# Kernel optimization log

Hardware: AMD Instinct MI355X
Metric: run time of the kernel (lower is better)

Reference implementation:

```python
import jax, jax.numpy as jnp
import numpy as np

S, H, NUM_TAG, D_LEN, MAX_LEN = 256, 1024, 20, 10, 1000


def setup_inputs() -> dict:
    key = jax.random.key(0)
    ks = jax.random.split(key, 6)
    sc = lambda d: 1.0 / np.sqrt(d)
    return {
        "hidden": jax.random.normal(ks[0], (S, H), jnp.float32),
        "target": jax.random.randint(ks[1], (S,), 0, NUM_TAG),
        "attn_w1": jax.random.normal(ks[2], (H, H), jnp.float32) * sc(H),
        "attn_b1": jnp.zeros((H,), jnp.float32),
        "attn_w2": jax.random.normal(ks[3], (H, 1), jnp.float32) * sc(H),
        "attn_b2": jnp.zeros((1,), jnp.float32),
        "len_emb": jax.random.normal(ks[4], (MAX_LEN, D_LEN), jnp.float32),
        "fc_w": jax.random.normal(ks[5], (3 * H + D_LEN, NUM_TAG), jnp.float32) * sc(3 * H + D_LEN),
        "fc_b": jnp.zeros((NUM_TAG,), jnp.float32),
    }


def reference(hidden, target, attn_w1, attn_b1, attn_w2, attn_b2, len_emb, fc_w, fc_b):
    S_, H_ = hidden.shape
    # attention scores [S]
    a = (jnp.tanh(hidden @ attn_w1 + attn_b1) @ attn_w2 + attn_b2)[:, 0]
    # prefix sums for contiguous-window softmax pooling
    e = jnp.exp(a - jnp.max(a))                                   # [S]
    Zc = jnp.concatenate([jnp.zeros((1,), e.dtype), jnp.cumsum(e)])                      # [S+1]
    Pc = jnp.concatenate([jnp.zeros((1, H_), e.dtype), jnp.cumsum(e[:, None] * hidden, axis=0)])  # [S+1,H]
    ii, jj = jnp.triu_indices(S_, k=1)                            # all spans i<j, loop order
    span = (Pc[jj + 1] - Pc[ii]) / (Zc[jj + 1] - Zc[ii])[:, None]  # softmax-weighted pooling
    lemb = len_emb[jj - ii + 1]                                   # segment length embedding (no grad in torch)
    feats = jnp.concatenate([span, hidden[ii], hidden[jj], lemb], axis=-1)  # [P, 3H+10]
    logits = feats @ fc_w + fc_b                                  # [P, num_tag]
    # is_span labels via run ids
    change = jnp.concatenate([jnp.array([True]), target[1:] != target[:-1]])
    run_id = jnp.cumsum(change.astype(jnp.int32))
    start = change
    end = jnp.concatenate([target[:-1] != target[1:], jnp.array([True])])
    labels = jnp.where((run_id[ii] == run_id[jj]) & start[ii] & end[jj], target[jj], 0)
    logp = jax.nn.log_softmax(logits, axis=-1)
    loss = -jnp.mean(jnp.take_along_axis(logp, labels[:, None].astype(jnp.int32), axis=1))
    return logits, loss.reshape(1)
```

## Files before the change

### kernel.cpp

```cpp
#include <hip/hip_runtime.h>
#include <math.h>

#define S 256
#define H 1024
#define NTAG 20
#define NPAIR 32640

#define WS_T     0
#define WS_A     2097152
#define WS_E     2097408
#define WS_ZC    2097664
#define WS_HW0   2097924
#define WS_HW1   2103044
#define WS_HW2   2108164
#define WS_PW    2113284
#define WS_LW    2118424
#define WS_LOSSP 2123564
#define WS_RUN   2123820
#define WS_START 2124076
#define WS_END   2124332

__global__ __launch_bounds__(256) void kA1(const float* __restrict__ hidden,
                                           const float* __restrict__ w1,
                                           float* __restrict__ ws) {
    const int tid = threadIdx.x;
    const int cg = blockIdx.x;
    const int rg = blockIdx.y;
    const int kc = blockIdx.z;

    __shared__ __align__(16) float shH[128][16];

    const int kk = tid & 127;
    const int r0 = (tid >> 7) * 8;
    #pragma unroll
    for (int e = 0; e < 8; e++)
        shH[kk][r0 + e] = hidden[(rg * 16 + r0 + e) * H + kc * 128 + kk];
    __syncthreads();

    float acc[16];
    #pragma unroll
    for (int r = 0; r < 16; r++) acc[r] = 0.f;

    const float* wp = w1 + (size_t)(kc * 128) * H + cg * 256 + tid;
    #pragma unroll 4
    for (int k = 0; k < 128; k++) {
        const float wv = wp[k * H];
        const float4 h0 = *(const float4*)&shH[k][0];
        const float4 h1 = *(const float4*)&shH[k][4];
        const float4 h2 = *(const float4*)&shH[k][8];
        const float4 h3 = *(const float4*)&shH[k][12];
        acc[0]  = fmaf(h0.x, wv, acc[0]);  acc[1]  = fmaf(h0.y, wv, acc[1]);
        acc[2]  = fmaf(h0.z, wv, acc[2]);  acc[3]  = fmaf(h0.w, wv, acc[3]);
        acc[4]  = fmaf(h1.x, wv, acc[4]);  acc[5]  = fmaf(h1.y, wv, acc[5]);
        acc[6]  = fmaf(h1.z, wv, acc[6]);  acc[7]  = fmaf(h1.w, wv, acc[7]);
        acc[8]  = fmaf(h2.x, wv, acc[8]);  acc[9]  = fmaf(h2.y, wv, acc[9]);
        acc[10] = fmaf(h2.z, wv, acc[10]); acc[11] = fmaf(h2.w, wv, acc[11]);
        acc[12] = fmaf(h3.x, wv, acc[12]); acc[13] = fmaf(h3.y, wv, acc[13]);
        acc[14] = fmaf(h3.z, wv, acc[14]); acc[15] = fmaf(h3.w, wv, acc[15]);
    }

    float* op = ws + WS_T + kc * (S * H) + (rg * 16) * H + cg * 256 + tid;
    #pragma unroll
    for (int r = 0; r < 16; r++) op[r * H] = acc[r];
}

__global__ __launch_bounds__(256) void kA2C(const float* __restrict__ hidden,
                                            const float* __restrict__ b1,
                                            const float* __restrict__ w2,
                                            const float* __restrict__ fcw,
                                            const float* __restrict__ lenemb,
                                            float* __restrict__ ws) {
    const int b = blockIdx.x;
    const int tid = threadIdx.x;
    if (b < 256) {
        __shared__ float hrow[1024];
        __shared__ float part[12][20];
        __shared__ float sred[256];

        #pragma unroll
        for (int e = 0; e < 4; e++)
            hrow[tid + e * 256] = hidden[b * H + tid + e * 256];

        float lacc = 0.f;
        #pragma unroll
        for (int q = 0; q < 4; q++) {
            const int c = q * 256 + tid;
            float sum = 0.f;
            #pragma unroll
            for (int kcz = 0; kcz < 8; kcz++)
                sum += ws[WS_T + kcz * (S * H) + b * H + c];
            lacc += tanhf(sum + b1[c]) * w2[c];
        }
        sred[tid] = lacc;
        __syncthreads();
        for (int off = 128; off > 0; off >>= 1) {
            if (tid < off) sred[tid] += sred[tid + off];
            __syncthreads();
        }
        if (tid == 0) ws[WS_A + b] = sred[0];

        if (tid < 240) {
            const int t = tid % 20, g = tid / 20;
            const int p = g >> 2, kc = g & 3;
            const float* fw = fcw + ((p << 10) + (kc << 8)) * 20 + t;
            const float* hr = hrow + (kc << 8);
            float sacc = 0.f;
            #pragma unroll 8
            for (int k = 0; k < 256; k++) sacc = fmaf(hr[k], fw[k * 20], sacc);
            part[g][t] = sacc;
        }
        __syncthreads();
        if (tid < 60) {
            const int t = tid % 20, p = tid / 20;
            const float v = part[p * 4 + 0][t] + part[p * 4 + 1][t] +
                            part[p * 4 + 2][t] + part[p * 4 + 3][t];
            const int base = (p == 0) ? WS_HW0 : (p == 1) ? WS_HW1 : WS_HW2;
            ws[base + b * 20 + t] = v;
        }
    } else {
        for (int item = tid; item < 255 * 20; item += 256) {
            const int L = 2 + item / 20;
            const int t = item % 20;
            float v = 0.f;
            #pragma unroll
            for (int d = 0; d < 10; d++)
                v = fmaf(lenemb[L * 10 + d], fcw[(3072 + d) * 20 + t], v);
            ws[WS_LW + L * 20 + t] = v;
        }
    }
}

__global__ __launch_bounds__(256) void kBD(const float* __restrict__ b2,
                                           const int* __restrict__ target,
                                           float* __restrict__ ws) {
    const int s = threadIdx.x;
    __shared__ float shf[256];
    __shared__ float she[256];
    __shared__ int   shi[256];
    __shared__ int   shtg[256];
    __shared__ float shw0[5120];

    shtg[s] = target[s];
    const float a = ws[WS_A + s] + b2[0];
    shf[s] = a;
    __syncthreads();
    for (int off = 128; off > 0; off >>= 1) {
        if (s < off) shf[s] = fmaxf(shf[s], shf[s + off]);
        __syncthreads();
    }
    const float mx = shf[0];
    __syncthreads();
    const float ev = expf(a - mx);
    she[s] = ev;
    ws[WS_E + s] = ev;
    shf[s] = ev;
    const int chg = (s == 0) ? 1 : (shtg[s] != shtg[s - 1]);
    shi[s] = chg;
    __syncthreads();
    for (int off = 1; off < 256; off <<= 1) {
        const float fv = (s >= off) ? shf[s - off] : 0.f;
        const int   iv = (s >= off) ? shi[s - off] : 0;
        __syncthreads();
        shf[s] += fv;
        shi[s] += iv;
        __syncthreads();
    }
    ws[WS_ZC + s + 1] = shf[s];
    if (s == 0) ws[WS_ZC] = 0.f;
    ((int*)ws)[WS_RUN + s]   = shi[s];
    ((int*)ws)[WS_START + s] = chg;
    ((int*)ws)[WS_END + s]   = (s == 255) ? 1 : (shtg[s] != shtg[s + 1]);
    for (int idx = s; idx < 5120; idx += 256) shw0[idx] = ws[WS_HW0 + idx];
    __syncthreads();
    if (s < 20) {
        float pw = 0.f;
        ws[WS_PW + s] = 0.f;
        for (int s2 = 0; s2 < 256; s2++) {
            pw = fmaf(she[s2], shw0[s2 * 20 + s], pw);
            ws[WS_PW + (s2 + 1) * 20 + s] = pw;
        }
    }
}

__global__ __launch_bounds__(256) void kE(const int* __restrict__ target,
                                          const float* __restrict__ fcb,
                                          float* __restrict__ out,
                                          float* __restrict__ ws) {
    const int i = blockIdx.x;
    const int j = threadIdx.x;
    __shared__ float sPwi[20], shw1i[20], sfcb[20];
    __shared__ float sred[256];

    if (j < 20) {
        sPwi[j]  = ws[WS_PW + i * 20 + j];
        shw1i[j] = ws[WS_HW1 + i * 20 + j];
        sfcb[j]  = fcb[j];
    }
    __syncthreads();

    const int* runid = (const int*)ws + WS_RUN;
    const int* stA   = (const int*)ws + WS_START;
    const int* enA   = (const int*)ws + WS_END;

    float lossacc = 0.f;
    if (j > i) {
        const float Zci  = ws[WS_ZC + i];
        const float invz = 1.f / (ws[WS_ZC + j + 1] - Zci);
        const int L = j - i + 1;
        const int lbl = (runid[i] == runid[j] && stA[i] && enA[j]) ? target[j] : 0;

        float pwv[20], h2v[20], lwv[20];
        const float4* pw4 = (const float4*)(ws + WS_PW + (j + 1) * 20);
        const float4* h24 = (const float4*)(ws + WS_HW2 + j * 20);
        const float4* lw4 = (const float4*)(ws + WS_LW + L * 20);
        #pragma unroll
        for (int q = 0; q < 5; q++) {
            float4 a = pw4[q], b = h24[q], cc = lw4[q];
            pwv[q*4+0]=a.x; pwv[q*4+1]=a.y; pwv[q*4+2]=a.z; pwv[q*4+3]=a.w;
            h2v[q*4+0]=b.x; h2v[q*4+1]=b.y; h2v[q*4+2]=b.z; h2v[q*4+3]=b.w;
            lwv[q*4+0]=cc.x; lwv[q*4+1]=cc.y; lwv[q*4+2]=cc.z; lwv[q*4+3]=cc.w;
        }

        float lg[20];
        float mx = -1e30f, chosen = 0.f;
        #pragma unroll
        for (int t = 0; t < 20; t++) {
            const float v = (pwv[t] - sPwi[t]) * invz + shw1i[t] + h2v[t] + lwv[t] + sfcb[t];
            lg[t] = v;
            mx = fmaxf(mx, v);
            chosen = (t == lbl) ? v : chosen;
        }
        const int p = i * 255 - (i * (i - 1)) / 2 + (j - i - 1);
        float4* op4 = (float4*)(out + (size_t)p * 20);
        #pragma unroll
        for (int q = 0; q < 5; q++)
            op4[q] = make_float4(lg[q*4+0], lg[q*4+1], lg[q*4+2], lg[q*4+3]);

        float se = 0.f;
        #pragma unroll
        for (int t = 0; t < 20; t++) se += expf(lg[t] - mx);
        lossacc = -(chosen - mx - logf(se));
    }
    sred[j] = lossacc;
    __syncthreads();
    for (int off = 128; off > 0; off >>= 1) {
        if (j < off) sred[j] += sred[j + off];
        __syncthreads();
    }
    if (j == 0) ws[WS_LOSSP + i] = sred[0];
}

__global__ __launch_bounds__(256) void kF(float* __restrict__ out,
                                          float* __restrict__ ws) {
    __shared__ float sh[256];
    const int t = threadIdx.x;
    sh[t] = (t < 255) ? ws[WS_LOSSP + t] : 0.f;
    __syncthreads();
    for (int off = 128; off > 0; off >>= 1) {
        if (t < off) sh[t] += sh[t + off];
        __syncthreads();
    }
    if (t == 0) out[(size_t)NPAIR * 20] = sh[0] / (float)NPAIR;
}

extern "C" void kernel_launch(void* const* d_in, const int* in_sizes, int n_in,
                              void* d_out, int out_size, void* d_ws, size_t ws_size,
                              hipStream_t stream) {
    (void)in_sizes; (void)n_in; (void)out_size; (void)ws_size;
    const float* hidden = (const float*)d_in[0];
    const int*   target = (const int*)d_in[1];
    const float* w1     = (const float*)d_in[2];
    const float* b1     = (const float*)d_in[3];
    const float* w2     = (const float*)d_in[4];
    const float* b2     = (const float*)d_in[5];
    const float* lenemb = (const float*)d_in[6];
    const float* fcw    = (const float*)d_in[7];
    const float* fcb    = (const float*)d_in[8];
    float* out = (float*)d_out;
    float* ws  = (float*)d_ws;

    kA1<<<dim3(4, 16, 8), 256, 0, stream>>>(hidden, w1, ws);
    kA2C<<<257, 256, 0, stream>>>(hidden, b1, w2, fcw, lenemb, ws);
    kBD<<<1, 256, 0, stream>>>(b2, target, ws);
    kE<<<255, 256, 0, stream>>>(target, fcb, out, ws);
    kF<<<1, 256, 0, stream>>>(out, ws);
}
```

Measured before the change: 44.34 us.

## Move fc-weight projections into GEMM kernel and flatten pair grid

The hidden·fc_w projections move out of the per-row reduction kernel into extra blocks of the W1 GEMM kernel. Those blocks write split-K partials that the reduction kernel then sums. The length-embedding projection moves into the single-block scan kernel. The pair-logit kernel now maps one thread per pair over 128 dense blocks, recovering (i,j) with a sqrt-based inverse, instead of 255 triangular blocks in which about half the threads sat idle. The intent is better load balance and less serial work between the GEMM and the scan, at the cost of an extra partial-sum buffer and index arithmetic per pair.

```diff
diff --git a/kernel.cpp b/kernel.cpp
--- a/kernel.cpp
+++ b/kernel.cpp
@@ -7,138 +7,145 @@
 #define NPAIR 32640
 
 #define WS_T     0
-#define WS_A     2097152
-#define WS_E     2097408
-#define WS_ZC    2097664
-#define WS_HW0   2097924
-#define WS_HW1   2103044
-#define WS_HW2   2108164
-#define WS_PW    2113284
-#define WS_LW    2118424
-#define WS_LOSSP 2123564
-#define WS_RUN   2123820
-#define WS_START 2124076
-#define WS_END   2124332
-
-__global__ __launch_bounds__(256) void kA1(const float* __restrict__ hidden,
-                                           const float* __restrict__ w1,
-                                           float* __restrict__ ws) {
+#define WS_HP    2097152
+#define WS_A     2220032
+#define WS_ZC    2220544
+#define WS_HW0   2220804
+#define WS_HW1   2225924
+#define WS_HW2   2231044
+#define WS_PW    2236164
+#define WS_LW    2241304
+#define WS_LOSSP 2246444
+#define WS_RUN   2246572
+#define WS_START 2246828
+#define WS_END   2247084
+
+__global__ __launch_bounds__(256) void kG(const float* __restrict__ hidden,
+                                          const float* __restrict__ w1,
+                                          const float* __restrict__ fcw,
+                                          float* __restrict__ ws) {
     const int tid = threadIdx.x;
-    const int cg = blockIdx.x;
-    const int rg = blockIdx.y;
-    const int kc = blockIdx.z;
-
-    __shared__ __align__(16) float shH[128][16];
-
-    const int kk = tid & 127;
-    const int r0 = (tid >> 7) * 8;
-    #pragma unroll
-    for (int e = 0; e < 8; e++)
-        shH[kk][r0 + e] = hidden[(rg * 16 + r0 + e) * H + kc * 128 + kk];
-    __syncthreads();
-
-    float acc[16];
-    #pragma unroll
-    for (int r = 0; r < 16; r++) acc[r] = 0.f;
-
-    const float* wp = w1 + (size_t)(kc * 128) * H + cg * 256 + tid;
-    #pragma unroll 4
-    for (int k = 0; k < 128; k++) {
-        const float wv = wp[k * H];
-        const float4 h0 = *(const float4*)&shH[k][0];
-        const float4 h1 = *(const float4*)&shH[k][4];
-        const float4 h2 = *(const float4*)&shH[k][8];
-        const float4 h3 = *(const float4*)&shH[k][12];
-        acc[0]  = fmaf(h0.x, wv, acc[0]);  acc[1]  = fmaf(h0.y, wv, acc[1]);
-        acc[2]  = fmaf(h0.z, wv, acc[2]);  acc[3]  = fmaf(h0.w, wv, acc[3]);
-        acc[4]  = fmaf(h1.x, wv, acc[4]);  acc[5]  = fmaf(h1.y, wv, acc[5]);
-        acc[6]  = fmaf(h1.z, wv, acc[6]);  acc[7]  = fmaf(h1.w, wv, acc[7]);
-        acc[8]  = fmaf(h2.x, wv, acc[8]);  acc[9]  = fmaf(h2.y, wv, acc[9]);
-        acc[10] = fmaf(h2.z, wv, acc[10]); acc[11] = fmaf(h2.w, wv, acc[11]);
-        acc[12] = fmaf(h3.x, wv, acc[12]); acc[13] = fmaf(h3.y, wv, acc[13]);
-        acc[14] = fmaf(h3.z, wv, acc[14]); acc[15] = fmaf(h3.w, wv, acc[15]);
-    }
-
-    float* op = ws + WS_T + kc * (S * H) + (rg * 16) * H + cg * 256 + tid;
-    #pragma unroll
-    for (int r = 0; r < 16; r++) op[r * H] = acc[r];
-}
-
-__global__ __launch_bounds__(256) void kA2C(const float* __restrict__ hidden,
-                                            const float* __restrict__ b1,
-                                            const float* __restrict__ w2,
-                                            const float* __restrict__ fcw,
-                                            const float* __restrict__ lenemb,
-                                            float* __restrict__ ws) {
     const int b = blockIdx.x;
-    const int tid = threadIdx.x;
-    if (b < 256) {
-        __shared__ float hrow[1024];
-        __shared__ float part[12][20];
-        __shared__ float sred[256];
-
-        #pragma unroll
-        for (int e = 0; e < 4; e++)
-            hrow[tid + e * 256] = hidden[b * H + tid + e * 256];
-
-        float lacc = 0.f;
-        #pragma unroll
-        for (int q = 0; q < 4; q++) {
-            const int c = q * 256 + tid;
-            float sum = 0.f;
+    __shared__ __align__(16) float shbuf[128 * 20];
+
+    if (b < 512) {
+        const int cg = b & 3, rg = (b >> 2) & 15, kc = b >> 6;
+        float (*shH)[20] = (float(*)[20])shbuf;
+        const int kk = tid & 127;
+        const int r0 = (tid >> 7) * 8;
+        #pragma unroll
+        for (int e = 0; e < 8; e++)
+            shH[kk][r0 + e] = hidden[(rg * 16 + r0 + e) * H + kc * 128 + kk];
+        __syncthreads();
+
+        float acc[16];
+        #pragma unroll
+        for (int r = 0; r < 16; r++) acc[r] = 0.f;
+
+        const float* wp = w1 + (size_t)(kc * 128) * H + cg * 256 + tid;
+        #pragma unroll 4
+        for (int k = 0; k < 128; k++) {
+            const float wv = wp[k * H];
+            const float4 h0 = *(const float4*)&shH[k][0];
+            const float4 h1 = *(const float4*)&shH[k][4];
+            const float4 h2 = *(const float4*)&shH[k][8];
+            const float4 h3 = *(const float4*)&shH[k][12];
+            acc[0]  = fmaf(h0.x, wv, acc[0]);  acc[1]  = fmaf(h0.y, wv, acc[1]);
+            acc[2]  = fmaf(h0.z, wv, acc[2]);  acc[3]  = fmaf(h0.w, wv, acc[3]);
+            acc[4]  = fmaf(h1.x, wv, acc[4]);  acc[5]  = fmaf(h1.y, wv, acc[5]);
+            acc[6]  = fmaf(h1.z, wv, acc[6]);  acc[7]  = fmaf(h1.w, wv, acc[7]);
+            acc[8]  = fmaf(h2.x, wv, acc[8]);  acc[9]  = fmaf(h2.y, wv, acc[9]);
+            acc[10] = fmaf(h2.z, wv, acc[10]); acc[11] = fmaf(h2.w, wv, acc[11]);
+            acc[12] = fmaf(h3.x, wv, acc[12]); acc[13] = fmaf(h3.y, wv, acc[13]);
+            acc[14] = fmaf(h3.z, wv, acc[14]); acc[15] = fmaf(h3.w, wv, acc[15]);
+        }
+        float* op = ws + WS_T + kc * (S * H) + (rg * 16) * H + cg * 256 + tid;
+        #pragma unroll
+        for (int r = 0; r < 16; r++) op[r * H] = acc[r];
+    } else {
+        const int hb = b - 512;
+        const int rg = hb & 15, kc = hb >> 4;
+        float (*shHT)[17] = (float(*)[17])shbuf;
+        {
+            const int c = tid & 127, rr = tid >> 7;
             #pragma unroll
-            for (int kcz = 0; kcz < 8; kcz++)
-                sum += ws[WS_T + kcz * (S * H) + b * H + c];
-            lacc += tanhf(sum + b1[c]) * w2[c];
-        }
-        sred[tid] = lacc;
-        __syncthreads();
-        for (int off = 128; off > 0; off >>= 1) {
-            if (tid < off) sred[tid] += sred[tid + off];
-            __syncthreads();
-        }
-        if (tid == 0) ws[WS_A + b] = sred[0];
-
+            for (int e = 0; e < 8; e++) {
+                const int r = e * 2 + rr;
+                shHT[c][r] = hidden[(rg * 16 + r) * H + kc * 128 + c];
+            }
+        }
+        __syncthreads();
         if (tid < 240) {
             const int t = tid % 20, g = tid / 20;
-            const int p = g >> 2, kc = g & 3;
-            const float* fw = fcw + ((p << 10) + (kc << 8)) * 20 + t;
-            const float* hr = hrow + (kc << 8);
-            float sacc = 0.f;
+            const int p = g >> 2, rsub = g & 3;
+            const float* fw = fcw + (size_t)(p * H + kc * 128) * 20 + t;
+            float a0 = 0.f, a1 = 0.f, a2 = 0.f, a3 = 0.f;
             #pragma unroll 8
-            for (int k = 0; k < 256; k++) sacc = fmaf(hr[k], fw[k * 20], sacc);
-            part[g][t] = sacc;
-        }
-        __syncthreads();
-        if (tid < 60) {
-            const int t = tid % 20, p = tid / 20;
-            const float v = part[p * 4 + 0][t] + part[p * 4 + 1][t] +
-                            part[p * 4 + 2][t] + part[p * 4 + 3][t];
-            const int base = (p == 0) ? WS_HW0 : (p == 1) ? WS_HW1 : WS_HW2;
-            ws[base + b * 20 + t] = v;
-        }
-    } else {
-        for (int item = tid; item < 255 * 20; item += 256) {
-            const int L = 2 + item / 20;
-            const int t = item % 20;
-            float v = 0.f;
-            #pragma unroll
-            for (int d = 0; d < 10; d++)
-                v = fmaf(lenemb[L * 10 + d], fcw[(3072 + d) * 20 + t], v);
-            ws[WS_LW + L * 20 + t] = v;
-        }
-    }
-}
-
-__global__ __launch_bounds__(256) void kBD(const float* __restrict__ b2,
-                                           const int* __restrict__ target,
-                                           float* __restrict__ ws) {
+            for (int k = 0; k < 128; k++) {
+                const float w = fw[k * 20];
+                a0 = fmaf(shHT[k][rsub * 4 + 0], w, a0);
+                a1 = fmaf(shHT[k][rsub * 4 + 1], w, a1);
+                a2 = fmaf(shHT[k][rsub * 4 + 2], w, a2);
+                a3 = fmaf(shHT[k][rsub * 4 + 3], w, a3);
+            }
+            float* hp = ws + WS_HP + ((size_t)(kc * 3 + p) * 256 + rg * 16 + rsub * 4) * 20 + t;
+            hp[0]  = a0; hp[20] = a1; hp[40] = a2; hp[60] = a3;
+        }
+    }
+}
+
+__global__ __launch_bounds__(256) void kR(const float* __restrict__ b1,
+                                          const float* __restrict__ w2,
+                                          float* __restrict__ ws) {
+    const int b = blockIdx.x, tid = threadIdx.x;
+    __shared__ float sred[256];
+    float lacc = 0.f;
+    #pragma unroll
+    for (int q = 0; q < 4; q++) {
+        const int c = q * 256 + tid;
+        float sum = 0.f;
+        #pragma unroll
+        for (int kcz = 0; kcz < 8; kcz++)
+            sum += ws[WS_T + kcz * (S * H) + b * H + c];
+        lacc += tanhf(sum + b1[c]) * w2[c];
+    }
+    sred[tid] = lacc;
+    __syncthreads();
+    for (int off = 128; off > 0; off >>= 1) {
+        if (tid < off) sred[tid] += sred[tid + off];
+        __syncthreads();
+    }
+    if (tid == 0) ws[WS_A + b] = sred[0];
+
+    if (tid < 60) {
+        const int t = tid % 20, p = tid / 20;
+        float s = 0.f;
+        #pragma unroll
+        for (int kc = 0; kc < 8; kc++)
+            s += ws[WS_HP + ((size_t)(kc * 3 + p) * 256 + b) * 20 + t];
+        const int base = (p == 0) ? WS_HW0 : (p == 1) ? WS_HW1 : WS_HW2;
+        ws[base + b * 20 + t] = s;
+    }
+}
+
+__global__ __launch_bounds__(256) void kS(const float* __restrict__ b2,
+                                          const int* __restrict__ target,
+                                          const float* __restrict__ lenemb,
+                                          const float* __restrict__ fcw,
+                                          float* __restrict__ ws) {
     const int s = threadIdx.x;
-    __shared__ float shf[256];
-    __shared__ float she[256];
-    __shared__ int   shi[256];
-    __shared__ int   shtg[256];
+    __shared__ float shf[256], she[256];
+    __shared__ int shi[256], shtg[256];
     __shared__ float shw0[5120];
+
+    for (int item = s; item < 255 * 20; item += 256) {
+        const int L = 2 + item / 20, t = item % 20;
+        float v = 0.f;
+        #pragma unroll
+        for (int d = 0; d < 10; d++)
+            v = fmaf(lenemb[L * 10 + d], fcw[(3072 + d) * 20 + t], v);
+        ws[WS_LW + L * 20 + t] = v;
+    }
 
     shtg[s] = target[s];
     const float a = ws[WS_A + s] + b2[0];
@@ -152,7 +159,6 @@
     __syncthreads();
     const float ev = expf(a - mx);
     she[s] = ev;
-    ws[WS_E + s] = ev;
     shf[s] = ev;
     const int chg = (s == 0) ? 1 : (shtg[s] != shtg[s - 1]);
     shi[s] = chg;
@@ -170,6 +176,7 @@
     ((int*)ws)[WS_RUN + s]   = shi[s];
     ((int*)ws)[WS_START + s] = chg;
     ((int*)ws)[WS_END + s]   = (s == 255) ? 1 : (shtg[s] != shtg[s + 1]);
+
     for (int idx = s; idx < 5120; idx += 256) shw0[idx] = ws[WS_HW0 + idx];
     __syncthreads();
     if (s < 20) {
@@ -186,77 +193,74 @@
                                           const float* __restrict__ fcb,
                                           float* __restrict__ out,
                                           float* __restrict__ ws) {
-    const int i = blockIdx.x;
-    const int j = threadIdx.x;
-    __shared__ float sPwi[20], shw1i[20], sfcb[20];
+    const int tid = threadIdx.x;
+    const int p = blockIdx.x * 256 + tid;
     __shared__ float sred[256];
-
-    if (j < 20) {
-        sPwi[j]  = ws[WS_PW + i * 20 + j];
-        shw1i[j] = ws[WS_HW1 + i * 20 + j];
-        sfcb[j]  = fcb[j];
-    }
-    __syncthreads();
-
-    const int* runid = (const int*)ws + WS_RUN;
-    const int* stA   = (const int*)ws + WS_START;
-    const int* enA   = (const int*)ws + WS_END;
-
     float lossacc = 0.f;
-    if (j > i) {
+    if (p < NPAIR) {
+        int i = (int)((511.0f - sqrtf((float)(261121 - 8 * p))) * 0.5f);
+        while ((i + 1) * (510 - i) <= 2 * p) ++i;
+        while (i > 0 && i * (511 - i) > 2 * p) --i;
+        const int j = p - i * (511 - i) / 2 + i + 1;
+
         const float Zci  = ws[WS_ZC + i];
         const float invz = 1.f / (ws[WS_ZC + j + 1] - Zci);
         const int L = j - i + 1;
+        const int* runid = (const int*)ws + WS_RUN;
+        const int* stA   = (const int*)ws + WS_START;
+        const int* enA   = (const int*)ws + WS_END;
         const int lbl = (runid[i] == runid[j] && stA[i] && enA[j]) ? target[j] : 0;
 
-        float pwv[20], h2v[20], lwv[20];
-        const float4* pw4 = (const float4*)(ws + WS_PW + (j + 1) * 20);
-        const float4* h24 = (const float4*)(ws + WS_HW2 + j * 20);
-        const float4* lw4 = (const float4*)(ws + WS_LW + L * 20);
-        #pragma unroll
-        for (int q = 0; q < 5; q++) {
-            float4 a = pw4[q], b = h24[q], cc = lw4[q];
-            pwv[q*4+0]=a.x; pwv[q*4+1]=a.y; pwv[q*4+2]=a.z; pwv[q*4+3]=a.w;
-            h2v[q*4+0]=b.x; h2v[q*4+1]=b.y; h2v[q*4+2]=b.z; h2v[q*4+3]=b.w;
-            lwv[q*4+0]=cc.x; lwv[q*4+1]=cc.y; lwv[q*4+2]=cc.z; lwv[q*4+3]=cc.w;
-        }
+        const float4* pwj4 = (const float4*)(ws + WS_PW + (j + 1) * 20);
+        const float4* pwi4 = (const float4*)(ws + WS_PW + i * 20);
+        const float4* h14  = (const float4*)(ws + WS_HW1 + i * 20);
+        const float4* h24  = (const float4*)(ws + WS_HW2 + j * 20);
+        const float4* lw4  = (const float4*)(ws + WS_LW + L * 20);
+        const float4* fb4  = (const float4*)fcb;
+        float4* op4 = (float4*)(out + (size_t)p * 20);
 
         float lg[20];
         float mx = -1e30f, chosen = 0.f;
         #pragma unroll
-        for (int t = 0; t < 20; t++) {
-            const float v = (pwv[t] - sPwi[t]) * invz + shw1i[t] + h2v[t] + lwv[t] + sfcb[t];
-            lg[t] = v;
-            mx = fmaxf(mx, v);
-            chosen = (t == lbl) ? v : chosen;
-        }
-        const int p = i * 255 - (i * (i - 1)) / 2 + (j - i - 1);
-        float4* op4 = (float4*)(out + (size_t)p * 20);
-        #pragma unroll
-        for (int q = 0; q < 5; q++)
-            op4[q] = make_float4(lg[q*4+0], lg[q*4+1], lg[q*4+2], lg[q*4+3]);
-
+        for (int q = 0; q < 5; q++) {
+            const float4 aj = pwj4[q], ai = pwi4[q];
+            const float4 bi = h14[q],  bj = h24[q];
+            const float4 cl = lw4[q],  fb = fb4[q];
+            float4 r;
+            r.x = (aj.x - ai.x) * invz + bi.x + bj.x + cl.x + fb.x;
+            r.y = (aj.y - ai.y) * invz + bi.y + bj.y + cl.y + fb.y;
+            r.z = (aj.z - ai.z) * invz + bi.z + bj.z + cl.z + fb.z;
+            r.w = (aj.w - ai.w) * invz + bi.w + bj.w + cl.w + fb.w;
+            op4[q] = r;
+            lg[q * 4 + 0] = r.x; lg[q * 4 + 1] = r.y;
+            lg[q * 4 + 2] = r.z; lg[q * 4 + 3] = r.w;
+            mx = fmaxf(mx, fmaxf(fmaxf(r.x, r.y), fmaxf(r.z, r.w)));
+            chosen = (q * 4 + 0 == lbl) ? r.x : chosen;
+            chosen = (q * 4 + 1 == lbl) ? r.y : chosen;
+            chosen = (q * 4 + 2 == lbl) ? r.z : chosen;
+            chosen = (q * 4 + 3 == lbl) ? r.w : chosen;
+        }
         float se = 0.f;
         #pragma unroll
         for (int t = 0; t < 20; t++) se += expf(lg[t] - mx);
         lossacc = -(chosen - mx - logf(se));
     }
-    sred[j] = lossacc;
+    sred[tid] = lossacc;
     __syncthreads();
     for (int off = 128; off > 0; off >>= 1) {
-        if (j < off) sred[j] += sred[j + off];
-        __syncthreads();
-    }
-    if (j == 0) ws[WS_LOSSP + i] = sred[0];
-}
-
-__global__ __launch_bounds__(256) void kF(float* __restrict__ out,
-                                          float* __restrict__ ws) {
-    __shared__ float sh[256];
+        if (tid < off) sred[tid] += sred[tid + off];
+        __syncthreads();
+    }
+    if (tid == 0) ws[WS_LOSSP + blockIdx.x] = sred[0];
+}
+
+__global__ __launch_bounds__(128) void kF(float* __restrict__ out,
+                                          float* __restrict__ ws) {
+    __shared__ float sh[128];
     const int t = threadIdx.x;
-    sh[t] = (t < 255) ? ws[WS_LOSSP + t] : 0.f;
-    __syncthreads();
-    for (int off = 128; off > 0; off >>= 1) {
+    sh[t] = ws[WS_LOSSP + t];
+    __syncthreads();
+    for (int off = 64; off > 0; off >>= 1) {
         if (t < off) sh[t] += sh[t + off];
         __syncthreads();
     }
@@ -279,9 +283,9 @@
     float* out = (float*)d_out;
     float* ws  = (float*)d_ws;
 
-    kA1<<<dim3(4, 16, 8), 256, 0, stream>>>(hidden, w1, ws);
-    kA2C<<<257, 256, 0, stream>>>(hidden, b1, w2, fcw, lenemb, ws);
-    kBD<<<1, 256, 0, stream>>>(b2, target, ws);
-    kE<<<255, 256, 0, stream>>>(target, fcb, out, ws);
-    kF<<<1, 256, 0, stream>>>(out, ws);
-}
+    kG<<<640, 256, 0, stream>>>(hidden, w1, fcw, ws);
+    kR<<<256, 256, 0, stream>>>(b1, w2, ws);
+    kS<<<1, 256, 0, stream>>>(b2, target, lenemb, fcw, ws);
+    kE<<<128, 256, 0, stream>>>(target, fcb, out, ws);
+    kF<<<1, 128, 0, stream>>>(out, ws);
+}
```

Result: no change. 44.67 us (+0.7%).
